# Kernel tuning notes

Hardware: AMD Instinct MI355X
Metric: run time of the kernel (lower is better)

Reference implementation:

```python
import jax, jax.numpy as jnp
import numpy as np

EPS = 1e-5  # BatchNorm2d default eps


def conv1x1_bn(x, W, gamma, beta, mean, var):
    # 1x1 conv (no bias) + BatchNorm2d in inference form.
    # x: (n, Cin, h, w), W: (Cout, Cin)
    y = jnp.einsum('oc,nchw->nohw', W, x)
    inv = gamma / jnp.sqrt(var + EPS)          # (C,)
    return y * inv[None, :, None, None] + (beta - mean * inv)[None, :, None, None]


def setup_inputs() -> dict:
    key = jax.random.key(0)
    ks = jax.random.split(key, 16)
    B, C, H, W = 8, 256, 128, 128
    sd = 1.0 / np.sqrt(C)
    inp = {
        'x':  jax.random.normal(ks[0], (B, C, H, W), jnp.float32),
        'Wk': jax.random.normal(ks[1], (C, C), jnp.float32) * sd,
        'k_gamma': jax.random.uniform(ks[2], (C,), jnp.float32, 0.5, 1.5),
        'k_beta':  jax.random.normal(ks[3], (C,), jnp.float32) * 0.1,
        'k_mean':  jax.random.normal(ks[4], (C,), jnp.float32) * 0.1,
        'k_var':   jax.random.uniform(ks[5], (C,), jnp.float32, 0.5, 1.5),
        'Wq': jax.random.normal(ks[6], (C, C), jnp.float32) * sd,
        'q_gamma': jax.random.uniform(ks[7], (C,), jnp.float32, 0.5, 1.5),
        'q_beta':  jax.random.normal(ks[8], (C,), jnp.float32) * 0.1,
        'q_mean':  jax.random.normal(ks[9], (C,), jnp.float32) * 0.1,
        'q_var':   jax.random.uniform(ks[10], (C,), jnp.float32, 0.5, 1.5),
        'Wv': jax.random.normal(ks[11], (C, C), jnp.float32) * sd,
        'v_gamma': jax.random.uniform(ks[12], (C,), jnp.float32, 0.5, 1.5),
        'v_beta':  jax.random.normal(ks[13], (C,), jnp.float32) * 0.1,
        'v_mean':  jax.random.normal(ks[14], (C,), jnp.float32) * 0.1,
        'v_var':   jax.random.uniform(ks[15], (C,), jnp.float32, 0.5, 1.5),
    }
    return inp


def reference(x, Wk, k_gamma, k_beta, k_mean, k_var,
              Wq, q_gamma, q_beta, q_mean, q_var,
              Wv, v_gamma, v_beta, v_mean, v_var):
    n, c, h, w = x.shape
    k = conv1x1_bn(x, Wk, k_gamma, k_beta, k_mean, k_var).reshape(n, c, h * w)  # (n,C,S)
    q = conv1x1_bn(x, Wq, q_gamma, q_beta, q_mean, q_var).reshape(n, c, h * w)
    v = conv1x1_bn(x, Wv, v_gamma, v_beta, v_mean, v_var).reshape(n, c, h * w)
    # torch: attention = softmax(q @ k^T, dim=2) -> (n, C, C) channel attention
    attn = jax.nn.softmax(jnp.einsum('ncs,nds->ncd', q, k), axis=-1)
    out = jnp.einsum('ncd,nds->ncs', attn, v).reshape(n, c, h, w)
    return out + x  # res = Identity (in_channels == out_channels)
```

## Files before the change

kernel.cpp:

```cpp
#include <hip/hip_runtime.h>


typedef __bf16 bf16x8 __attribute__((ext_vector_type(8)));
typedef float f32x4 __attribute__((ext_vector_type(4)));
typedef unsigned short us8 __attribute__((ext_vector_type(8)));

#define EPS 1e-5f

__device__ __forceinline__ unsigned short f2bf(float f) {
  unsigned int u = __float_as_uint(f);
  u += 0x7fffu + ((u >> 16) & 1u);
  return (unsigned short)(u >> 16);
}
__device__ __forceinline__ float bf2f(unsigned short h) {
  return __uint_as_float(((unsigned int)h) << 16);
}
__device__ __forceinline__ bf16x8 ld_frag(const unsigned short* p) {
  union { us8 u; bf16x8 b; } x;
  x.u = *(const us8*)p;
  return x.b;
}

#define LDB 72

#define CONV_WRITE(dst)                                                     \
  _Pragma("unroll")                                                         \
  for (int u = 0; u < 4; ++u) {                                             \
    float fv[8] = {pa[u].x, pa[u].y, pa[u].z, pa[u].w,                      \
                   pb[u].x, pb[u].y, pb[u].z, pb[u].w};                     \
    union { unsigned short s[8]; uint4 v; } H, L;                           \
    _Pragma("unroll")                                                       \
    for (int e = 0; e < 8; ++e) {                                           \
      const unsigned short h = f2bf(fv[e]);                                 \
      H.s[e] = h;                                                           \
      L.s[e] = f2bf(2.0f * (fv[e] - bf2f(h)));                              \
      rs[u] += fv[e];                                                       \
    }                                                                       \
    *(uint4*)&sh[dst][(srow + u * 64) * LDB + sg * 8] = H.v;                \
    *(uint4*)&sl[dst][(srow + u * 64) * LDB + sg * 8] = L.v;                \
  }

__global__ __launch_bounds__(512, 2) void kGram(const float* __restrict__ x,
                                                float* __restrict__ Gp,
                                                float* __restrict__ rp,
                                                int chunk) {
  __shared__ __align__(16) unsigned short sh[2][256 * LDB];
  __shared__ __align__(16) unsigned short sl[2][256 * LDB];
  const int n = blockIdx.y;
  const int k0 = blockIdx.x * chunk;
  const int nkt = chunk >> 6;
  const int tid = threadIdx.x;
  const float* xn = x + (size_t)n * 4194304;

  f32x4 acc[4][8];
  const f32x4 z4 = {0.f, 0.f, 0.f, 0.f};
#pragma unroll
  for (int i = 0; i < 4; ++i)
#pragma unroll
    for (int j = 0; j < 8; ++j) acc[i][j] = z4;
  float rs[4] = {0.f, 0.f, 0.f, 0.f};

  const int lane = tid & 63, w = tid >> 6;
  const int m = lane & 15, q = lane >> 4;
  const int wr = w >> 1, wc = w & 1;
  const int srow = tid >> 3, sg = tid & 7;

  float4 pa[4], pb[4];

#pragma unroll
  for (int u = 0; u < 4; ++u) {
    const float* p = xn + (size_t)(srow + u * 64) * 16384 + k0 + sg * 8;
    pa[u] = *(const float4*)p;
    pb[u] = *(const float4*)(p + 4);
  }
  CONV_WRITE(0)
  __syncthreads();

  for (int kt = 0; kt < nkt; ++kt) {
    const int b = kt & 1;
    const bool more = (kt + 1 < nkt);
    if (more) {
      const int kb = k0 + (kt + 1) * 64;
#pragma unroll
      for (int u = 0; u < 4; ++u) {
        const float* p = xn + (size_t)(srow + u * 64) * 16384 + kb + sg * 8;
        pa[u] = *(const float4*)p;
        pb[u] = *(const float4*)(p + 4);
      }
    }
#pragma unroll
    for (int kk = 0; kk < 64; kk += 32) {
      bf16x8 Ah[4];
#pragma unroll
      for (int i = 0; i < 4; ++i)
        Ah[i] = ld_frag(&sh[b][(wr * 64 + i * 16 + m) * LDB + kk + q * 8]);
#pragma unroll
      for (int j = 0; j < 8; ++j) {
        const int off = (wc * 128 + j * 16 + m) * LDB + kk + q * 8;
        const bf16x8 Bh = ld_frag(&sh[b][off]);
        const bf16x8 Bl = ld_frag(&sl[b][off]);
#pragma unroll
        for (int i = 0; i < 4; ++i) {
          acc[i][j] = __builtin_amdgcn_mfma_f32_16x16x32_bf16(Ah[i], Bh, acc[i][j], 0, 0, 0);
          acc[i][j] = __builtin_amdgcn_mfma_f32_16x16x32_bf16(Ah[i], Bl, acc[i][j], 0, 0, 0);
        }
      }
    }
    if (more) {
      const int nb = b ^ 1;
      CONV_WRITE(nb)
      __syncthreads();
    }
  }

  const size_t slot = (size_t)n * gridDim.x + blockIdx.x;
#pragma unroll
  for (int u = 0; u < 4; ++u) {
    float v = rs[u];
    v += __shfl_xor(v, 1);
    v += __shfl_xor(v, 2);
    v += __shfl_xor(v, 4);
    if ((lane & 7) == 0) rp[slot * 256 + (srow + u * 64)] = v;
  }
  float* Gpn = Gp + slot * 65536;
#pragma unroll
  for (int i = 0; i < 4; ++i)
#pragma unroll
    for (int j = 0; j < 8; ++j)
#pragma unroll
      for (int e = 0; e < 4; ++e) {
        const int grow = wr * 64 + i * 16 + q * 4 + e;
        const int gcol = wc * 128 + j * 16 + m;
        Gpn[grow * 256 + gcol] = 0.5f * acc[i][j][e];
      }
}

__global__ void kReduce(float* __restrict__ Gp, int splits) {
  const int e4 = (blockIdx.x * 256 + threadIdx.x) * 4;
  const int n = e4 >> 16, el = e4 & 65535;
  float* p = Gp + (size_t)n * splits * 65536 + el;
  float4 s = {0.f, 0.f, 0.f, 0.f};
  for (int i = 0; i < splits; ++i) {
    const float4 v = *(const float4*)(p + (size_t)i * 65536);
    s.x += v.x; s.y += v.y; s.z += v.z; s.w += v.w;
  }
  *(float4*)p = s;
}

__global__ void kSym(const float* __restrict__ Gs, float* __restrict__ G,
                     int sstride) {
  __shared__ __align__(16) float pt[64][68];
  const int n = blockIdx.y;
  const int bi = blockIdx.x >> 2, bj = blockIdx.x & 3;
  const float* gsn = Gs + (size_t)n * sstride;
  float* gn = G + (size_t)n * 65536;
  const int t = threadIdx.x, r = t >> 2, cg = (t & 3) * 16;
#pragma unroll
  for (int e = 0; e < 16; e += 4)
    *(float4*)&pt[r][cg + e] =
        *(const float4*)(gsn + (size_t)(bj * 64 + r) * 256 + bi * 64 + cg + e);
  __syncthreads();
#pragma unroll
  for (int e = 0; e < 16; e += 4) {
    const float4 a =
        *(const float4*)(gsn + (size_t)(bi * 64 + r) * 256 + bj * 64 + cg + e);
    float4 o;
    o.x = a.x + pt[cg + e + 0][r];
    o.y = a.y + pt[cg + e + 1][r];
    o.z = a.z + pt[cg + e + 2][r];
    o.w = a.w + pt[cg + e + 3][r];
    *(float4*)(gn + (size_t)(bi * 64 + r) * 256 + bj * 64 + cg + e) = o;
  }
}

#define TLD 260
__global__ __launch_bounds__(256) void kAttn(
    const float* __restrict__ G, const float* __restrict__ rp, int splits,
    const float* __restrict__ Wq, const float* __restrict__ qga, const float* __restrict__ qbe,
    const float* __restrict__ qme, const float* __restrict__ qva,
    const float* __restrict__ Wk, const float* __restrict__ kga, const float* __restrict__ kbe,
    const float* __restrict__ kme, const float* __restrict__ kva,
    const float* __restrict__ Wv, const float* __restrict__ vga, const float* __restrict__ vbe,
    const float* __restrict__ vme, const float* __restrict__ vva,
    unsigned short* __restrict__ M, float* __restrict__ cvec) {
  __shared__ __align__(16) float t_lds[8 * TLD];
  __shared__ __align__(16) float p_lds[8 * TLD];
  __shared__ __align__(16) float r_lds[256];
  __shared__ float ivv_lds[256], bv_lds[256];
  __shared__ float rq_lds[8], bq_lds[8], rsum_lds[8];

  const int n = blockIdx.y, r0 = blockIdx.x * 8;
  const int t = threadIdx.x;
  const int lane = t & 63;
  const int w = __builtin_amdgcn_readfirstlane(t >> 6);
  const float* Gn = G + (size_t)n * 65536;

  {
    float s = 0.f;
    const float* p = rp + (size_t)n * splits * 256 + t;
    for (int ss = 0; ss < splits; ++ss) s += p[ss * 256];
    r_lds[t] = s;
    const float iv = vga[t] * rsqrtf(vva[t] + EPS);
    ivv_lds[t] = iv;
    bv_lds[t] = vbe[t] - vme[t] * iv;
  }
  __syncthreads();

  const int c0 = r0 + 2 * w, c1 = c0 + 1;
  const float ivq0 = qga[c0] * rsqrtf(qva[c0] + EPS);
  const float ivq1 = qga[c1] * rsqrtf(qva[c1] + EPS);

  {
    const float4 r4 = *(const float4*)(r_lds + lane * 4);
#pragma unroll
    for (int rr = 0; rr < 2; ++rr) {
      const float4 w4 = *(const float4*)(Wq + (size_t)(c0 + rr) * 256 + lane * 4);
      float s = w4.x * r4.x + w4.y * r4.y + w4.z * r4.z + w4.w * r4.w;
      s += __shfl_xor(s, 1);  s += __shfl_xor(s, 2);  s += __shfl_xor(s, 4);
      s += __shfl_xor(s, 8);  s += __shfl_xor(s, 16); s += __shfl_xor(s, 32);
      if (lane == 0) rq_lds[2 * w + rr] = s * (rr ? ivq1 : ivq0);
    }
    if (lane == 0) {
      bq_lds[2 * w + 0] = qbe[c0] - qme[c0] * ivq0;
      bq_lds[2 * w + 1] = qbe[c1] - qme[c1] * ivq1;
    }
  }

  {
    float4 tr0 = {0.f, 0.f, 0.f, 0.f}, tr1 = {0.f, 0.f, 0.f, 0.f};
    const float* wq0 = Wq + (size_t)c0 * 256;
    const float* wq1 = Wq + (size_t)c1 * 256;
    for (int kb = 0; kb < 256; kb += 4) {
      union { float4 v; float f[4]; } A0, A1;
      A0.v = *(const float4*)(wq0 + kb);
      A1.v = *(const float4*)(wq1 + kb);
#pragma unroll
      for (int e = 0; e < 4; ++e) {
        const float4 g4 = *(const float4*)(Gn + (size_t)(kb + e) * 256 + lane * 4);
        const float a0 = A0.f[e], a1 = A1.f[e];
        tr0.x += a0 * g4.x; tr0.y += a0 * g4.y; tr0.z += a0 * g4.z; tr0.w += a0 * g4.w;
        tr1.x += a1 * g4.x; tr1.y += a1 * g4.y; tr1.z += a1 * g4.z; tr1.w += a1 * g4.w;
      }
    }
    tr0.x *= ivq0; tr0.y *= ivq0; tr0.z *= ivq0; tr0.w *= ivq0;
    tr1.x *= ivq1; tr1.y *= ivq1; tr1.z *= ivq1; tr1.w *= ivq1;
    *(float4*)(t_lds + (2 * w + 0) * TLD + lane * 4) = tr0;
    *(float4*)(t_lds + (2 * w + 1) * TLD + lane * 4) = tr1;
  }
  __syncthreads();

  {
    float lreg[8];
#pragma unroll
    for (int i = 0; i < 8; ++i) lreg[i] = 0.f;
    const float ivk = kga[t] * rsqrtf(kva[t] + EPS);
    const float bkd = kbe[t] - kme[t] * ivk;
    float rkd = 0.f;
    const float* wkrow = Wk + (size_t)t * 256;
    for (int jb = 0; jb < 256; jb += 4) {
      const float4 w4 = *(const float4*)(wkrow + jb);
      const float4 r4 = *(const float4*)(r_lds + jb);
      rkd += w4.x * r4.x + w4.y * r4.y + w4.z * r4.z + w4.w * r4.w;
#pragma unroll
      for (int i = 0; i < 8; ++i) {
        const float4 t4 = *(const float4*)(t_lds + i * TLD + jb);
        lreg[i] += t4.x * w4.x + t4.y * w4.y + t4.z * w4.z + t4.w * w4.w;
      }
    }
#pragma unroll
    for (int i = 0; i < 8; ++i)
      p_lds[i * TLD + t] = ivk * lreg[i] + rq_lds[i] * bkd +
                           bq_lds[i] * (ivk * rkd) + 16384.0f * bq_lds[i] * bkd;
  }
  __syncthreads();

  {
    const int i = t >> 5, s = t & 31;
    float* row = p_lds + i * TLD;
    float mx = -1e30f;
#pragma unroll
    for (int u = 0; u < 8; ++u) mx = fmaxf(mx, row[s + u * 32]);
    mx = fmaxf(mx, __shfl_xor(mx, 1));
    mx = fmaxf(mx, __shfl_xor(mx, 2));
    mx = fmaxf(mx, __shfl_xor(mx, 4));
    mx = fmaxf(mx, __shfl_xor(mx, 8));
    mx = fmaxf(mx, __shfl_xor(mx, 16));
    float sraw = 0.f, sbv = 0.f;
#pragma unroll
    for (int u = 0; u < 8; ++u) {
      const int d = s + u * 32;
      const float e = __expf(row[d] - mx);
      sraw += e;
      sbv += e * bv_lds[d];
      row[d] = e * ivv_lds[d];
    }
    sraw += __shfl_xor(sraw, 1);  sbv += __shfl_xor(sbv, 1);
    sraw += __shfl_xor(sraw, 2);  sbv += __shfl_xor(sbv, 2);
    sraw += __shfl_xor(sraw, 4);  sbv += __shfl_xor(sbv, 4);
    sraw += __shfl_xor(sraw, 8);  sbv += __shfl_xor(sbv, 8);
    sraw += __shfl_xor(sraw, 16); sbv += __shfl_xor(sbv, 16);
    if (s == 0) {
      rsum_lds[i] = sraw;
      cvec[n * 256 + r0 + i] = sbv / sraw;
    }
  }
  __syncthreads();

  {
    float mreg[8];
#pragma unroll
    for (int i = 0; i < 8; ++i) mreg[i] = 0.f;
    for (int db = 0; db < 256; db += 4) {
      float wv[4];
#pragma unroll
      for (int e = 0; e < 4; ++e) wv[e] = Wv[(size_t)(db + e) * 256 + t];
#pragma unroll
      for (int i = 0; i < 8; ++i) {
        const float4 p4 = *(const float4*)(p_lds + i * TLD + db);
        mreg[i] += p4.x * wv[0] + p4.y * wv[1] + p4.z * wv[2] + p4.w * wv[3];
      }
    }
#pragma unroll
    for (int i = 0; i < 8; ++i)
      M[((size_t)n * 256 + r0 + i) * 256 + t] = f2bf(mreg[i] / rsum_lds[i]);
  }
}

#define LDT 40
__global__ __launch_bounds__(256, 2) void kOut(const float* __restrict__ x,
                                               const unsigned short* __restrict__ M,
                                               const float* __restrict__ cvec,
                                               float* __restrict__ out) {
  __shared__ __align__(16) unsigned short xt[64 * LDT];
  __shared__ __align__(16) float xf[256 * 64];
  const int n = blockIdx.y, s0 = blockIdx.x * 64;
  const int tid = threadIdx.x;
  const float* xn = x + (size_t)n * 4194304;
  const unsigned short* Mn = M + (size_t)n * 65536;
  const int lane = tid & 63, w = tid >> 6;
  const int m = lane & 15, q = lane >> 4;

  f32x4 acc[4][4];
  const f32x4 z4 = {0.f, 0.f, 0.f, 0.f};
#pragma unroll
  for (int i = 0; i < 4; ++i)
#pragma unroll
    for (int ct = 0; ct < 4; ++ct) acc[i][ct] = z4;

  for (int kt = 0; kt < 8; ++kt) {
    __syncthreads();
#pragma unroll
    for (int u = 0; u < 2; ++u) {
      const int fidx = tid + u * 256;
      const int ch = fidx >> 4, f = fidx & 15;
      const float4 v = *(const float4*)(xn + (size_t)(kt * 32 + ch) * 16384 + s0 + f * 4);
      *(float4*)&xf[(kt * 32 + ch) * 64 + f * 4] = v;
      xt[(f * 4 + 0) * LDT + ch] = f2bf(v.x);
      xt[(f * 4 + 1) * LDT + ch] = f2bf(v.y);
      xt[(f * 4 + 2) * LDT + ch] = f2bf(v.z);
      xt[(f * 4 + 3) * LDT + ch] = f2bf(v.w);
    }
    __syncthreads();
    bf16x8 A[4], B[4];
#pragma unroll
    for (int i = 0; i < 4; ++i)
      A[i] = ld_frag(&Mn[((w * 4 + i) * 16 + m) * 256 + kt * 32 + q * 8]);
#pragma unroll
    for (int ct = 0; ct < 4; ++ct)
      B[ct] = ld_frag(&xt[(ct * 16 + m) * LDT + q * 8]);
#pragma unroll
    for (int i = 0; i < 4; ++i)
#pragma unroll
      for (int ct = 0; ct < 4; ++ct)
        acc[i][ct] = __builtin_amdgcn_mfma_f32_16x16x32_bf16(A[i], B[ct], acc[i][ct], 0, 0, 0);
  }
#pragma unroll
  for (int i = 0; i < 4; ++i) {
    const int cb = w * 64 + i * 16 + q * 4;
#pragma unroll
    for (int e = 0; e < 4; ++e) {
      const int c = cb + e;
      const float cv = cvec[n * 256 + c];
      float* orow = out + ((size_t)n * 256 + c) * 16384 + s0;
#pragma unroll
      for (int ct = 0; ct < 4; ++ct) {
        const int s = ct * 16 + m;
        orow[s] = acc[i][ct][e] + cv + xf[c * 64 + s];
      }
    }
  }
}

extern "C" void kernel_launch(void* const* d_in, const int* in_sizes, int n_in,
                              void* d_out, int out_size, void* d_ws, size_t ws_size,
                              hipStream_t stream) {
  const float* x   = (const float*)d_in[0];
  const float* Wk  = (const float*)d_in[1];
  const float* kga = (const float*)d_in[2];
  const float* kbe = (const float*)d_in[3];
  const float* kme = (const float*)d_in[4];
  const float* kva = (const float*)d_in[5];
  const float* Wq  = (const float*)d_in[6];
  const float* qga = (const float*)d_in[7];
  const float* qbe = (const float*)d_in[8];
  const float* qme = (const float*)d_in[9];
  const float* qva = (const float*)d_in[10];
  const float* Wv  = (const float*)d_in[11];
  const float* vga = (const float*)d_in[12];
  const float* vbe = (const float*)d_in[13];
  const float* vme = (const float*)d_in[14];
  const float* vva = (const float*)d_in[15];

  char* ws = (char*)d_ws;
  float* G           = (float*)(ws);
  unsigned short* Mm = (unsigned short*)(ws + 2097152);
  float* cv          = (float*)(ws + 3145728);
  float* rp          = (float*)(ws + 3153920);
  float* Gp          = (float*)(ws + 3416064);
  float* out         = (float*)d_out;

  int splits = 32;
  while (splits > 1 &&
         (size_t)3416064 + (size_t)splits * 8 * 65536 * 4 > ws_size)
    splits >>= 1;
  const int chunk = 16384 / splits;

  kGram<<<dim3(splits, 8), 512, 0, stream>>>(x, Gp, rp, chunk);
  kReduce<<<512, 256, 0, stream>>>(Gp, splits);
  kSym<<<dim3(16, 8), 256, 0, stream>>>(Gp, G, splits * 65536);
  kAttn<<<dim3(32, 8), 256, 0, stream>>>(G, rp, splits,
                                         Wq, qga, qbe, qme, qva,
                                         Wk, kga, kbe, kme, kva,
                                         Wv, vga, vbe, vme, vva,
                                         Mm, cv);
  kOut<<<dim3(256, 8), 256, 0, stream>>>(x, Mm, cv, out);
}
```

Before: 393.2 us.

## Split Gram kernel rows across two blocks and prefetch x in output kernel

The Gram kernel now launches two blocks per split, each computing half the output rows with 256 threads. The shared-memory tile shrinks to 32 columns, and single buffering plus an extra barrier replaces the old double buffer. Every block still loads and converts the full 256-channel tile, so x reads and bf16 conversion work double in exchange for more blocks and smaller LDS. The output kernel now register-prefetches the next x tile so global loads overlap the MFMA work.

```diff
diff --git a/kernel.cpp b/kernel.cpp
--- a/kernel.cpp
+++ b/kernel.cpp
@@ -21,9 +21,9 @@
   return x.b;
 }
 
-#define LDB 72
-
-#define CONV_WRITE(dst)                                                     \
+#define LDBS 40
+
+#define CONV_WRITE                                                          \
   _Pragma("unroll")                                                         \
   for (int u = 0; u < 4; ++u) {                                             \
     float fv[8] = {pa[u].x, pa[u].y, pa[u].z, pa[u].w,                      \
@@ -31,24 +31,24 @@
     union { unsigned short s[8]; uint4 v; } H, L;                           \
     _Pragma("unroll")                                                       \
     for (int e = 0; e < 8; ++e) {                                           \
-      const unsigned short h = f2bf(fv[e]);                                 \
-      H.s[e] = h;                                                           \
-      L.s[e] = f2bf(2.0f * (fv[e] - bf2f(h)));                              \
+      const unsigned short hh = f2bf(fv[e]);                                \
+      H.s[e] = hh;                                                          \
+      L.s[e] = f2bf(2.0f * (fv[e] - bf2f(hh)));                             \
       rs[u] += fv[e];                                                       \
     }                                                                       \
-    *(uint4*)&sh[dst][(srow + u * 64) * LDB + sg * 8] = H.v;                \
-    *(uint4*)&sl[dst][(srow + u * 64) * LDB + sg * 8] = L.v;                \
-  }
-
-__global__ __launch_bounds__(512, 2) void kGram(const float* __restrict__ x,
+    *(uint4*)&sh[(srow + u * 64) * LDBS + sg * 8] = H.v;                    \
+    *(uint4*)&sl[(srow + u * 64) * LDBS + sg * 8] = L.v;                    \
+  }
+
+__global__ __launch_bounds__(256, 2) void kGram(const float* __restrict__ x,
                                                 float* __restrict__ Gp,
                                                 float* __restrict__ rp,
                                                 int chunk) {
-  __shared__ __align__(16) unsigned short sh[2][256 * LDB];
-  __shared__ __align__(16) unsigned short sl[2][256 * LDB];
-  const int n = blockIdx.y;
+  __shared__ __align__(16) unsigned short sh[256 * LDBS];
+  __shared__ __align__(16) unsigned short sl[256 * LDBS];
+  const int n = blockIdx.z, h = blockIdx.y;
   const int k0 = blockIdx.x * chunk;
-  const int nkt = chunk >> 6;
+  const int nkt = chunk >> 5;
   const int tid = threadIdx.x;
   const float* xn = x + (size_t)n * 4194304;
 
@@ -63,7 +63,7 @@
   const int lane = tid & 63, w = tid >> 6;
   const int m = lane & 15, q = lane >> 4;
   const int wr = w >> 1, wc = w & 1;
-  const int srow = tid >> 3, sg = tid & 7;
+  const int srow = tid >> 2, sg = tid & 3;
 
   float4 pa[4], pb[4];
 
@@ -73,14 +73,13 @@
     pa[u] = *(const float4*)p;
     pb[u] = *(const float4*)(p + 4);
   }
-  CONV_WRITE(0)
-  __syncthreads();
 
   for (int kt = 0; kt < nkt; ++kt) {
-    const int b = kt & 1;
-    const bool more = (kt + 1 < nkt);
-    if (more) {
-      const int kb = k0 + (kt + 1) * 64;
+    if (kt) __syncthreads();
+    CONV_WRITE
+    __syncthreads();
+    if (kt + 1 < nkt) {
+      const int kb = k0 + (kt + 1) * 32;
 #pragma unroll
       for (int u = 0; u < 4; ++u) {
         const float* p = xn + (size_t)(srow + u * 64) * 16384 + kb + sg * 8;
@@ -88,39 +87,32 @@
         pb[u] = *(const float4*)(p + 4);
       }
     }
-#pragma unroll
-    for (int kk = 0; kk < 64; kk += 32) {
-      bf16x8 Ah[4];
-#pragma unroll
-      for (int i = 0; i < 4; ++i)
-        Ah[i] = ld_frag(&sh[b][(wr * 64 + i * 16 + m) * LDB + kk + q * 8]);
-#pragma unroll
-      for (int j = 0; j < 8; ++j) {
-        const int off = (wc * 128 + j * 16 + m) * LDB + kk + q * 8;
-        const bf16x8 Bh = ld_frag(&sh[b][off]);
-        const bf16x8 Bl = ld_frag(&sl[b][off]);
-#pragma unroll
-        for (int i = 0; i < 4; ++i) {
-          acc[i][j] = __builtin_amdgcn_mfma_f32_16x16x32_bf16(Ah[i], Bh, acc[i][j], 0, 0, 0);
-          acc[i][j] = __builtin_amdgcn_mfma_f32_16x16x32_bf16(Ah[i], Bl, acc[i][j], 0, 0, 0);
-        }
-      }
-    }
-    if (more) {
-      const int nb = b ^ 1;
-      CONV_WRITE(nb)
-      __syncthreads();
+    bf16x8 Ah[4];
+#pragma unroll
+    for (int i = 0; i < 4; ++i)
+      Ah[i] = ld_frag(&sh[(h * 128 + wr * 64 + i * 16 + m) * LDBS + q * 8]);
+#pragma unroll
+    for (int j = 0; j < 8; ++j) {
+      const int off = (wc * 128 + j * 16 + m) * LDBS + q * 8;
+      const bf16x8 Bh = ld_frag(&sh[off]);
+      const bf16x8 Bl = ld_frag(&sl[off]);
+#pragma unroll
+      for (int i = 0; i < 4; ++i) {
+        acc[i][j] = __builtin_amdgcn_mfma_f32_16x16x32_bf16(Ah[i], Bh, acc[i][j], 0, 0, 0);
+        acc[i][j] = __builtin_amdgcn_mfma_f32_16x16x32_bf16(Ah[i], Bl, acc[i][j], 0, 0, 0);
+      }
     }
   }
 
   const size_t slot = (size_t)n * gridDim.x + blockIdx.x;
-#pragma unroll
-  for (int u = 0; u < 4; ++u) {
-    float v = rs[u];
-    v += __shfl_xor(v, 1);
-    v += __shfl_xor(v, 2);
-    v += __shfl_xor(v, 4);
-    if ((lane & 7) == 0) rp[slot * 256 + (srow + u * 64)] = v;
+  if (h == 0) {
+#pragma unroll
+    for (int u = 0; u < 4; ++u) {
+      float v = rs[u];
+      v += __shfl_xor(v, 1);
+      v += __shfl_xor(v, 2);
+      if ((lane & 3) == 0) rp[slot * 256 + (srow + u * 64)] = v;
+    }
   }
   float* Gpn = Gp + slot * 65536;
 #pragma unroll
@@ -129,7 +121,7 @@
     for (int j = 0; j < 8; ++j)
 #pragma unroll
       for (int e = 0; e < 4; ++e) {
-        const int grow = wr * 64 + i * 16 + q * 4 + e;
+        const int grow = h * 128 + wr * 64 + i * 16 + q * 4 + e;
         const int gcol = wc * 128 + j * 16 + m;
         Gpn[grow * 256 + gcol] = 0.5f * acc[i][j][e];
       }
@@ -339,6 +331,7 @@
   const unsigned short* Mn = M + (size_t)n * 65536;
   const int lane = tid & 63, w = tid >> 6;
   const int m = lane & 15, q = lane >> 4;
+  const int ch0 = tid >> 4, f0 = tid & 15;
 
   f32x4 acc[4][4];
   const f32x4 z4 = {0.f, 0.f, 0.f, 0.f};
@@ -347,24 +340,34 @@
 #pragma unroll
     for (int ct = 0; ct < 4; ++ct) acc[i][ct] = z4;
 
+  float4 pv[2];
+#pragma unroll
+  for (int u = 0; u < 2; ++u)
+    pv[u] = *(const float4*)(xn + (size_t)(ch0 + u * 16) * 16384 + s0 + f0 * 4);
+
   for (int kt = 0; kt < 8; ++kt) {
-    __syncthreads();
+    if (kt) __syncthreads();
 #pragma unroll
     for (int u = 0; u < 2; ++u) {
-      const int fidx = tid + u * 256;
-      const int ch = fidx >> 4, f = fidx & 15;
-      const float4 v = *(const float4*)(xn + (size_t)(kt * 32 + ch) * 16384 + s0 + f * 4);
-      *(float4*)&xf[(kt * 32 + ch) * 64 + f * 4] = v;
-      xt[(f * 4 + 0) * LDT + ch] = f2bf(v.x);
-      xt[(f * 4 + 1) * LDT + ch] = f2bf(v.y);
-      xt[(f * 4 + 2) * LDT + ch] = f2bf(v.z);
-      xt[(f * 4 + 3) * LDT + ch] = f2bf(v.w);
-    }
-    __syncthreads();
-    bf16x8 A[4], B[4];
+      const int ch = kt * 32 + ch0 + u * 16;
+      const float4 v = pv[u];
+      *(float4*)&xf[ch * 64 + f0 * 4] = v;
+      xt[(f0 * 4 + 0) * LDT + ch - kt * 32] = f2bf(v.x);
+      xt[(f0 * 4 + 1) * LDT + ch - kt * 32] = f2bf(v.y);
+      xt[(f0 * 4 + 2) * LDT + ch - kt * 32] = f2bf(v.z);
+      xt[(f0 * 4 + 3) * LDT + ch - kt * 32] = f2bf(v.w);
+    }
+    bf16x8 A[4];
 #pragma unroll
     for (int i = 0; i < 4; ++i)
       A[i] = ld_frag(&Mn[((w * 4 + i) * 16 + m) * 256 + kt * 32 + q * 8]);
+    __syncthreads();
+    if (kt < 7) {
+#pragma unroll
+      for (int u = 0; u < 2; ++u)
+        pv[u] = *(const float4*)(xn + (size_t)((kt + 1) * 32 + ch0 + u * 16) * 16384 + s0 + f0 * 4);
+    }
+    bf16x8 B[4];
 #pragma unroll
     for (int ct = 0; ct < 4; ++ct)
       B[ct] = ld_frag(&xt[(ct * 16 + m) * LDT + q * 8]);
@@ -425,7 +428,7 @@
     splits >>= 1;
   const int chunk = 16384 / splits;
 
-  kGram<<<dim3(splits, 8), 512, 0, stream>>>(x, Gp, rp, chunk);
+  kGram<<<dim3(splits, 2, 8), 256, 0, stream>>>(x, Gp, rp, chunk);
   kReduce<<<512, 256, 0, stream>>>(Gp, splits);
   kSym<<<dim3(16, 8), 256, 0, stream>>>(Gp, G, splits * 65536);
   kAttn<<<dim3(32, 8), 256, 0, stream>>>(G, rp, splits,
```

Measured after the change: 388.1 us. Within noise of the previous version (-1.3%).
